# Kernel optimization log

Hardware: AMD Instinct MI355X
Metric: run time of the kernel (lower is better)

Reference implementation:

```python
import jax, jax.numpy as jnp
import numpy as np

D_IN = 2048
D_OUT = 2048
NUM_HEADS = 16
HEAD_DIM = D_OUT // NUM_HEADS
LATENT = 256
B, S = 2, 2048


def setup_inputs() -> dict:
    key = jax.random.key(0)
    ks = jax.random.split(key, 7)
    s = lambda fan_in: 1.0 / np.sqrt(fan_in)
    return {
        "x": jax.random.normal(ks[0], (B, S, D_IN), dtype=jnp.float32),
        "W_query": jax.random.normal(ks[1], (D_IN, D_OUT), dtype=jnp.float32) * s(D_IN),
        "W_DKV": jax.random.normal(ks[2], (D_IN, LATENT), dtype=jnp.float32) * s(D_IN),
        "W_UK": jax.random.normal(ks[3], (LATENT, D_OUT), dtype=jnp.float32) * s(LATENT),
        "W_UV": jax.random.normal(ks[4], (LATENT, D_OUT), dtype=jnp.float32) * s(LATENT),
        "W_out": jax.random.normal(ks[5], (D_OUT, D_OUT), dtype=jnp.float32) * s(D_OUT),
        "b_out": jax.random.normal(ks[6], (D_OUT,), dtype=jnp.float32) * 0.01,
    }


def reference(x, W_query, W_DKV, W_UK, W_UV, W_out, b_out):
    b, n, _ = x.shape
    # projections
    q = x @ W_query                      # [b, n, d_out]
    latent = x @ W_DKV                   # [b, n, latent]
    k = latent @ W_UK                    # [b, n, d_out]
    v = latent @ W_UV                    # [b, n, d_out]
    # split heads -> [b, h, n, hd]
    to_heads = lambda t: t.reshape(b, n, NUM_HEADS, HEAD_DIM).transpose(0, 2, 1, 3)
    q, k, v = to_heads(q), to_heads(k), to_heads(v)
    scores = jnp.einsum("bhqd,bhkd->bhqk", q, k)
    # causal mask: q_pos < k_pos masked to -inf (applied BEFORE scaling, as in source)
    qpos = jnp.arange(n)[:, None]
    kpos = jnp.arange(n)[None, :]
    scores = jnp.where(qpos < kpos, -jnp.inf, scores)
    attn = jax.nn.softmax(scores / np.sqrt(HEAD_DIM), axis=-1)
    ctx = jnp.einsum("bhqk,bhkd->bhqd", attn, v)   # [b, h, n, hd]
    ctx = ctx.transpose(0, 2, 1, 3).reshape(b, n, D_OUT)
    return ctx @ W_out + b_out
```

## Files before the change

### kernel.cpp

```cpp
#include <hip/hip_runtime.h>

#define DIN 2048
#define DOUT 2048
#define NHEADS 16
#define HDIM 128
#define LATENT 256
#define BB 2
#define SS 2048
#define MTOT (BB*SS)

using bf16 = __bf16;
using bf16x8 = __attribute__((ext_vector_type(8))) __bf16;
using f32x4 = __attribute__((ext_vector_type(4))) float;

__device__ __forceinline__ void gload16(const bf16* g, bf16* l) {
    __builtin_amdgcn_global_load_lds(
        (const __attribute__((address_space(1))) void*)g,
        (__attribute__((address_space(3))) void*)l, 16, 0, 0);
}

__global__ void cast_f32_bf16(const float* __restrict__ in, bf16* __restrict__ out, int n) {
    int i = (blockIdx.x * blockDim.x + threadIdx.x) * 8;
    if (i >= n) return;
    float4 a = *(const float4*)(in + i);
    float4 b = *(const float4*)(in + i + 4);
    bf16x8 o;
    o[0] = (bf16)a.x; o[1] = (bf16)a.y; o[2] = (bf16)a.z; o[3] = (bf16)a.w;
    o[4] = (bf16)b.x; o[5] = (bf16)b.y; o[6] = (bf16)b.z; o[7] = (bf16)b.w;
    *(bf16x8*)(out + i) = o;
}

__global__ void transpose_cast(const float* __restrict__ W, bf16* __restrict__ WT, int R, int C) {
    __shared__ float tile[32][33];
    int c0 = blockIdx.x * 32, r0 = blockIdx.y * 32;
    int tx = threadIdx.x & 31, ty = threadIdx.x >> 5;
    #pragma unroll
    for (int i = ty; i < 32; i += 8)
        tile[i][tx] = W[(size_t)(r0 + i) * C + c0 + tx];
    __syncthreads();
    #pragma unroll
    for (int i = ty; i < 32; i += 8)
        WT[(size_t)(c0 + i) * R + r0 + tx] = (bf16)tile[tx][i];
}

__global__ void transpose_v(const bf16* __restrict__ v, bf16* __restrict__ vT) {
    int bh = blockIdx.z;
    int s0 = blockIdx.x * 32, d0 = blockIdx.y * 32;
    __shared__ bf16 t[32][33];
    int tx = threadIdx.x & 31, ty = threadIdx.x >> 5;
    int b = bh >> 4, h = bh & 15;
    #pragma unroll
    for (int i = ty; i < 32; i += 8)
        t[i][tx] = v[(size_t)(b * SS + s0 + i) * DOUT + h * HDIM + d0 + tx];
    __syncthreads();
    #pragma unroll
    for (int i = ty; i < 32; i += 8)
        vT[((size_t)bh * HDIM + d0 + i) * SS + s0 + tx] = t[tx][i];
}

template<bool OUT_F32, bool BIAS>
__global__ __launch_bounds__(256) void gemm_bt(const bf16* __restrict__ A,
        const bf16* __restrict__ BT, void* __restrict__ Cp,
        const float* __restrict__ bias, const int Kdim, const int Ndim) {
    const int n0 = blockIdx.x * 128, m0 = blockIdx.y * 128;
    const int tid = threadIdx.x, wave = tid >> 6, lane = tid & 63;
    const int wm = wave >> 1, wn = wave & 1;
    const int lr = lane & 15, lg = lane >> 4;
    __shared__ __align__(16) bf16 As[128][32];
    __shared__ __align__(16) bf16 Bs[128][32];
    f32x4 acc[4][4];
    #pragma unroll
    for (int i = 0; i < 4; ++i)
        #pragma unroll
        for (int j = 0; j < 4; ++j) acc[i][j] = (f32x4){0.f, 0.f, 0.f, 0.f};

    const int sr = lane >> 2;
    const int sc = (lane & 3) * 8;
    const bf16* ga = A  + (size_t)(m0 + wave * 16 + sr) * Kdim + sc;
    const bf16* gb = BT + (size_t)(n0 + wave * 16 + sr) * Kdim + sc;
    const size_t stride64 = (size_t)64 * Kdim;
    bf16* lAd = &As[wave * 16][0];
    bf16* lBd = &Bs[wave * 16][0];

    for (int k0 = 0; k0 < Kdim; k0 += 32) {
        gload16(ga,            lAd);
        gload16(ga + stride64, lAd + 64 * 32);
        gload16(gb,            lBd);
        gload16(gb + stride64, lBd + 64 * 32);
        ga += 32; gb += 32;
        __syncthreads();
        bf16x8 af[4], bfr[4];
        #pragma unroll
        for (int i = 0; i < 4; ++i)
            af[i] = *(const bf16x8*)&As[wm * 64 + i * 16 + lr][lg * 8];
        #pragma unroll
        for (int j = 0; j < 4; ++j)
            bfr[j] = *(const bf16x8*)&Bs[wn * 64 + j * 16 + lr][lg * 8];
        #pragma unroll
        for (int i = 0; i < 4; ++i)
            #pragma unroll
            for (int j = 0; j < 4; ++j)
                acc[i][j] = __builtin_amdgcn_mfma_f32_16x16x32_bf16(af[i], bfr[j], acc[i][j], 0, 0, 0);
        __syncthreads();
    }
    #pragma unroll
    for (int i = 0; i < 4; ++i)
        #pragma unroll
        for (int j = 0; j < 4; ++j) {
            const int r0 = m0 + wm * 64 + i * 16 + lg * 4;
            const int c = n0 + wn * 64 + j * 16 + lr;
            #pragma unroll
            for (int r2 = 0; r2 < 4; ++r2) {
                float v = acc[i][j][r2];
                if (BIAS) v += bias[c];
                if (OUT_F32) ((float*)Cp)[(size_t)(r0 + r2) * Ndim + c] = v;
                else         ((bf16*)Cp)[(size_t)(r0 + r2) * Ndim + c] = (bf16)v;
            }
        }
}

__global__ __launch_bounds__(256) void attn_kernel(const bf16* __restrict__ q,
        const bf16* __restrict__ k, const bf16* __restrict__ vT, bf16* __restrict__ ctx) {
    const int bh = blockIdx.y, b = bh >> 4, h = bh & 15;
    const int tid = threadIdx.x, wave = tid >> 6, lane = tid & 63;
    const int lr = lane & 15, lg = lane >> 4;
    __shared__ __align__(16) bf16 Ks[64][HDIM + 8];
    __shared__ __align__(16) bf16 Vs[HDIM][64 + 8];
    __shared__ __align__(16) bf16 Ps[64][64 + 8];

    for (int half = 0; half < 2; ++half) {
        const int qt = half ? (31 - (int)blockIdx.x) : (int)blockIdx.x;
        const int q0 = qt * 64;

        bf16x8 qf[4];
        const bf16* qbase = q + ((size_t)(b * SS + q0 + wave * 16 + lr)) * DOUT + h * HDIM;
        #pragma unroll
        for (int d = 0; d < 4; ++d) qf[d] = *(const bf16x8*)(qbase + d * 32 + lg * 8);

        f32x4 o[8];
        #pragma unroll
        for (int i = 0; i < 8; ++i) o[i] = (f32x4){0.f, 0.f, 0.f, 0.f};
        float m_i[4], l_i[4];
        #pragma unroll
        for (int r = 0; r < 4; ++r) { m_i[r] = -__builtin_inff(); l_i[r] = 0.f; }
        const float scale = 0.088388347648318447f;

        const int nkt = qt + 1;
        for (int kt = 0; kt < nkt; ++kt) {
            const int kbase = kt * 64;
            {
                int krow = tid >> 2, kcs = (tid & 3) * 32;
                const bf16* gk = k + ((size_t)(b * SS + kbase + krow)) * DOUT + h * HDIM + kcs;
                #pragma unroll
                for (int u = 0; u < 4; ++u)
                    *(bf16x8*)&Ks[krow][kcs + u * 8] = *(const bf16x8*)(gk + u * 8);
                int vr = tid >> 1, vcs = (tid & 1) * 32;
                const bf16* gv = vT + ((size_t)bh * HDIM + vr) * SS + kbase + vcs;
                #pragma unroll
                for (int u = 0; u < 4; ++u)
                    *(bf16x8*)&Vs[vr][vcs + u * 8] = *(const bf16x8*)(gv + u * 8);
            }
            __syncthreads();

            f32x4 sacc[4];
            #pragma unroll
            for (int nf = 0; nf < 4; ++nf) sacc[nf] = (f32x4){0.f, 0.f, 0.f, 0.f};
            __builtin_amdgcn_s_setprio(1);
            #pragma unroll
            for (int nf = 0; nf < 4; ++nf)
                #pragma unroll
                for (int d = 0; d < 4; ++d) {
                    bf16x8 kf = *(const bf16x8*)&Ks[nf * 16 + lr][d * 32 + lg * 8];
                    sacc[nf] = __builtin_amdgcn_mfma_f32_16x16x32_bf16(qf[d], kf, sacc[nf], 0, 0, 0);
                }
            __builtin_amdgcn_s_setprio(0);

            float sv[4][4];
            const bool maskt = (kbase + 63 > q0);
            #pragma unroll
            for (int nf = 0; nf < 4; ++nf)
                #pragma unroll
                for (int r = 0; r < 4; ++r) {
                    float s = sacc[nf][r] * scale;
                    if (maskt) {
                        int qr = q0 + wave * 16 + lg * 4 + r;
                        int kc = kbase + nf * 16 + lr;
                        if (qr < kc) s = -__builtin_inff();
                    }
                    sv[nf][r] = s;
                }
            float corr[4];
            #pragma unroll
            for (int r = 0; r < 4; ++r) {
                float v = fmaxf(fmaxf(sv[0][r], sv[1][r]), fmaxf(sv[2][r], sv[3][r]));
                #pragma unroll
                for (int off = 1; off < 16; off <<= 1) v = fmaxf(v, __shfl_xor(v, off));
                float mnew = fmaxf(m_i[r], v);
                corr[r] = __expf(m_i[r] - mnew);
                m_i[r] = mnew;
            }
            float rsum[4] = {0.f, 0.f, 0.f, 0.f};
            #pragma unroll
            for (int nf = 0; nf < 4; ++nf)
                #pragma unroll
                for (int r = 0; r < 4; ++r) {
                    float p = __expf(sv[nf][r] - m_i[r]);
                    rsum[r] += p;
                    Ps[wave * 16 + lg * 4 + r][nf * 16 + lr] = (bf16)p;
                }
            #pragma unroll
            for (int r = 0; r < 4; ++r) {
                float v = rsum[r];
                #pragma unroll
                for (int off = 1; off < 16; off <<= 1) v += __shfl_xor(v, off);
                l_i[r] = l_i[r] * corr[r] + v;
            }
            #pragma unroll
            for (int df = 0; df < 8; ++df)
                #pragma unroll
                for (int r = 0; r < 4; ++r) o[df][r] *= corr[r];

            __builtin_amdgcn_s_setprio(1);
            #pragma unroll
            for (int ks = 0; ks < 2; ++ks) {
                bf16x8 pf = *(const bf16x8*)&Ps[wave * 16 + lr][ks * 32 + lg * 8];
                #pragma unroll
                for (int df = 0; df < 8; ++df) {
                    bf16x8 vf = *(const bf16x8*)&Vs[df * 16 + lr][ks * 32 + lg * 8];
                    o[df] = __builtin_amdgcn_mfma_f32_16x16x32_bf16(pf, vf, o[df], 0, 0, 0);
                }
            }
            __builtin_amdgcn_s_setprio(0);
            __syncthreads();
        }

        #pragma unroll
        for (int df = 0; df < 8; ++df)
            #pragma unroll
            for (int r = 0; r < 4; ++r) {
                int rrow = q0 + wave * 16 + lg * 4 + r;
                int col = h * HDIM + df * 16 + lr;
                ctx[(size_t)(b * SS + rrow) * DOUT + col] = (bf16)(o[df][r] / l_i[r]);
            }
    }
}

extern "C" void kernel_launch(void* const* d_in, const int* in_sizes, int n_in,
                              void* d_out, int out_size, void* d_ws, size_t ws_size,
                              hipStream_t stream) {
    const float* x    = (const float*)d_in[0];
    const float* Wq   = (const float*)d_in[1];
    const float* Wdkv = (const float*)d_in[2];
    const float* Wuk  = (const float*)d_in[3];
    const float* Wuv  = (const float*)d_in[4];
    const float* Wout = (const float*)d_in[5];
    const float* bout = (const float*)d_in[6];

    char* ws = (char*)d_ws;
    size_t off = 0;
    auto alloc = [&](size_t bytes) { char* p = ws + off; off = (off + bytes + 255) & ~255ULL; return p; };
    bf16* xb    = (bf16*)alloc((size_t)MTOT * DIN * 2);
    bf16* WqT   = (bf16*)alloc((size_t)DOUT * DIN * 2);
    bf16* WdkvT = (bf16*)alloc((size_t)LATENT * DIN * 2);
    bf16* WukT  = (bf16*)alloc((size_t)DOUT * LATENT * 2);
    bf16* WuvT  = (bf16*)alloc((size_t)DOUT * LATENT * 2);
    bf16* WoutT = (bf16*)alloc((size_t)DOUT * DOUT * 2);
    bf16* qb    = (bf16*)alloc((size_t)MTOT * DOUT * 2);
    bf16* lat   = (bf16*)alloc((size_t)MTOT * LATENT * 2);
    bf16* kb    = (bf16*)alloc((size_t)MTOT * DOUT * 2);
    bf16* vb    = (bf16*)alloc((size_t)MTOT * DOUT * 2);
    bf16* vT    = (bf16*)alloc((size_t)BB * NHEADS * HDIM * SS * 2);
    bf16* ctx   = (bf16*)alloc((size_t)MTOT * DOUT * 2);

    cast_f32_bf16<<<(MTOT * DIN) / 8 / 256, 256, 0, stream>>>(x, xb, MTOT * DIN);
    transpose_cast<<<dim3(DOUT / 32, DIN / 32), 256, 0, stream>>>(Wq, WqT, DIN, DOUT);
    transpose_cast<<<dim3(LATENT / 32, DIN / 32), 256, 0, stream>>>(Wdkv, WdkvT, DIN, LATENT);
    transpose_cast<<<dim3(DOUT / 32, LATENT / 32), 256, 0, stream>>>(Wuk, WukT, LATENT, DOUT);
    transpose_cast<<<dim3(DOUT / 32, LATENT / 32), 256, 0, stream>>>(Wuv, WuvT, LATENT, DOUT);
    transpose_cast<<<dim3(DOUT / 32, DOUT / 32), 256, 0, stream>>>(Wout, WoutT, DOUT, DOUT);

    gemm_bt<false, false><<<dim3(DOUT / 128, MTOT / 128), 256, 0, stream>>>(xb, WqT, qb, nullptr, DIN, DOUT);
    gemm_bt<false, false><<<dim3(LATENT / 128, MTOT / 128), 256, 0, stream>>>(xb, WdkvT, lat, nullptr, DIN, LATENT);
    gemm_bt<false, false><<<dim3(DOUT / 128, MTOT / 128), 256, 0, stream>>>(lat, WukT, kb, nullptr, LATENT, DOUT);
    gemm_bt<false, false><<<dim3(DOUT / 128, MTOT / 128), 256, 0, stream>>>(lat, WuvT, vb, nullptr, LATENT, DOUT);

    transpose_v<<<dim3(SS / 32, HDIM / 32, BB * NHEADS), 256, 0, stream>>>(vb, vT);

    attn_kernel<<<dim3(16, BB * NHEADS), 256, 0, stream>>>(qb, kb, vT, ctx);

    gemm_bt<true, true><<<dim3(DOUT / 128, MTOT / 128), 256, 0, stream>>>(ctx, WoutT, d_out, bout, DOUT, DOUT);
}
```

Measured before the change: 428.5 us.

## Fuse projection GEMMs, prefetch K/V in attention, swizzle LDS and block order

Merges the Q and latent projections into one GEMM, and the K and V up-projections into another, by relying on the transposed weights sitting contiguously in the workspace. The GEMM now takes separate leading dimensions so it can read and write the strided fused buffers. The attention kernel gains register prefetch of the next K/V tile, XOR-swizzled LDS layouts to avoid bank conflicts, and exp2 with the softmax scale folded in. Both kernels also remap block order with an XCD-style swizzle. The intent is fewer launches, better L2 locality and less LDS and latency stall, at the cost of relying on the workspace layout and on a finite -3e38 mask value.

```diff
diff --git a/kernel.cpp b/kernel.cpp
--- a/kernel.cpp
+++ b/kernel.cpp
@@ -8,6 +8,8 @@
 #define BB 2
 #define SS 2048
 #define MTOT (BB*SS)
+#define QLD (DOUT + LATENT)
+#define KLD (2*DOUT)
 
 using bf16 = __bf16;
 using bf16x8 = __attribute__((ext_vector_type(8))) __bf16;
@@ -51,7 +53,7 @@
     int b = bh >> 4, h = bh & 15;
     #pragma unroll
     for (int i = ty; i < 32; i += 8)
-        t[i][tx] = v[(size_t)(b * SS + s0 + i) * DOUT + h * HDIM + d0 + tx];
+        t[i][tx] = v[(size_t)(b * SS + s0 + i) * KLD + h * HDIM + d0 + tx];
     __syncthreads();
     #pragma unroll
     for (int i = ty; i < 32; i += 8)
@@ -61,8 +63,13 @@
 template<bool OUT_F32, bool BIAS>
 __global__ __launch_bounds__(256) void gemm_bt(const bf16* __restrict__ A,
         const bf16* __restrict__ BT, void* __restrict__ Cp,
-        const float* __restrict__ bias, const int Kdim, const int Ndim) {
-    const int n0 = blockIdx.x * 128, m0 = blockIdx.y * 128;
+        const float* __restrict__ bias, const int Kdim, const int Ald,
+        const int Ndim, const int Cld) {
+    const int nwg = gridDim.x * gridDim.y;
+    int orig = blockIdx.y * gridDim.x + blockIdx.x;
+    int swz = (orig & 7) * (nwg >> 3) + (orig >> 3);
+    const int n0 = (swz % gridDim.x) * 128, m0 = (swz / gridDim.x) * 128;
+
     const int tid = threadIdx.x, wave = tid >> 6, lane = tid & 63;
     const int wm = wave >> 1, wn = wave & 1;
     const int lr = lane & 15, lg = lane >> 4;
@@ -76,17 +83,18 @@
 
     const int sr = lane >> 2;
     const int sc = (lane & 3) * 8;
-    const bf16* ga = A  + (size_t)(m0 + wave * 16 + sr) * Kdim + sc;
+    const bf16* ga = A  + (size_t)(m0 + wave * 16 + sr) * Ald + sc;
     const bf16* gb = BT + (size_t)(n0 + wave * 16 + sr) * Kdim + sc;
-    const size_t stride64 = (size_t)64 * Kdim;
+    const size_t strideA64 = (size_t)64 * Ald;
+    const size_t strideB64 = (size_t)64 * Kdim;
     bf16* lAd = &As[wave * 16][0];
     bf16* lBd = &Bs[wave * 16][0];
 
     for (int k0 = 0; k0 < Kdim; k0 += 32) {
-        gload16(ga,            lAd);
-        gload16(ga + stride64, lAd + 64 * 32);
-        gload16(gb,            lBd);
-        gload16(gb + stride64, lBd + 64 * 32);
+        gload16(ga,             lAd);
+        gload16(ga + strideA64, lAd + 64 * 32);
+        gload16(gb,             lBd);
+        gload16(gb + strideB64, lBd + 64 * 32);
         ga += 32; gb += 32;
         __syncthreads();
         bf16x8 af[4], bfr[4];
@@ -113,27 +121,46 @@
             for (int r2 = 0; r2 < 4; ++r2) {
                 float v = acc[i][j][r2];
                 if (BIAS) v += bias[c];
-                if (OUT_F32) ((float*)Cp)[(size_t)(r0 + r2) * Ndim + c] = v;
-                else         ((bf16*)Cp)[(size_t)(r0 + r2) * Ndim + c] = (bf16)v;
+                if (OUT_F32) ((float*)Cp)[(size_t)(r0 + r2) * Cld + c] = v;
+                else         ((bf16*)Cp)[(size_t)(r0 + r2) * Cld + c] = (bf16)v;
             }
         }
 }
 
 __global__ __launch_bounds__(256) void attn_kernel(const bf16* __restrict__ q,
         const bf16* __restrict__ k, const bf16* __restrict__ vT, bf16* __restrict__ ctx) {
-    const int bh = blockIdx.y, b = bh >> 4, h = bh & 15;
+    int orig = blockIdx.y * 16 + blockIdx.x;
+    int swz = (orig & 7) * 64 + (orig >> 3);
+    const int bx = swz & 15, bh = swz >> 4;
+    const int b = bh >> 4, h = bh & 15;
     const int tid = threadIdx.x, wave = tid >> 6, lane = tid & 63;
     const int lr = lane & 15, lg = lane >> 4;
-    __shared__ __align__(16) bf16 Ks[64][HDIM + 8];
-    __shared__ __align__(16) bf16 Vs[HDIM][64 + 8];
-    __shared__ __align__(16) bf16 Ps[64][64 + 8];
+
+    __shared__ __align__(16) bf16 KsL[64 * 128];
+    __shared__ __align__(16) bf16 VsL[128 * 64];
+    __shared__ __align__(16) bf16 PsL[64 * 64];
+
+    char* KsB = (char*)KsL; char* VsB = (char*)VsL; char* PsB = (char*)PsL;
+
+    const int krow = tid >> 2, kc0b = (tid & 3) * 64;
+    const int vrow = tid >> 1, vc0b = (tid & 1) * 64;
+    int kOff[4], vOff[4];
+    #pragma unroll
+    for (int u = 0; u < 4; ++u) {
+        kOff[u] = (krow * 256 + kc0b + u * 16) ^ ((krow & 7) << 4);
+        vOff[u] = (vrow * 128 + vc0b + u * 16) ^ ((vrow & 7) << 4);
+    }
+    const bf16* gkb = k  + ((size_t)b * SS + krow) * KLD + h * HDIM + (tid & 3) * 32;
+    const bf16* gvb = vT + ((size_t)bh * HDIM + vrow) * SS + (tid & 1) * 32;
+
+    const float C = 0.12751744f;
 
     for (int half = 0; half < 2; ++half) {
-        const int qt = half ? (31 - (int)blockIdx.x) : (int)blockIdx.x;
+        const int qt = half ? (31 - bx) : bx;
         const int q0 = qt * 64;
 
         bf16x8 qf[4];
-        const bf16* qbase = q + ((size_t)(b * SS + q0 + wave * 16 + lr)) * DOUT + h * HDIM;
+        const bf16* qbase = q + ((size_t)(b * SS + q0 + wave * 16 + lr)) * QLD + h * HDIM;
         #pragma unroll
         for (int d = 0; d < 4; ++d) qf[d] = *(const bf16x8*)(qbase + d * 32 + lg * 8);
 
@@ -142,25 +169,34 @@
         for (int i = 0; i < 8; ++i) o[i] = (f32x4){0.f, 0.f, 0.f, 0.f};
         float m_i[4], l_i[4];
         #pragma unroll
-        for (int r = 0; r < 4; ++r) { m_i[r] = -__builtin_inff(); l_i[r] = 0.f; }
-        const float scale = 0.088388347648318447f;
+        for (int r = 0; r < 4; ++r) { m_i[r] = -3.0e38f; l_i[r] = 0.f; }
 
         const int nkt = qt + 1;
+        bf16x8 kreg[4], vreg[4];
+        #pragma unroll
+        for (int u = 0; u < 4; ++u) {
+            kreg[u] = *(const bf16x8*)(gkb + (size_t)0 * 64 * KLD + u * 8);
+            vreg[u] = *(const bf16x8*)(gvb + 0 * 64 + u * 8);
+        }
+        #pragma unroll
+        for (int u = 0; u < 4; ++u) {
+            *(bf16x8*)(KsB + kOff[u]) = kreg[u];
+            *(bf16x8*)(VsB + vOff[u]) = vreg[u];
+        }
+        __syncthreads();
+
         for (int kt = 0; kt < nkt; ++kt) {
             const int kbase = kt * 64;
-            {
-                int krow = tid >> 2, kcs = (tid & 3) * 32;
-                const bf16* gk = k + ((size_t)(b * SS + kbase + krow)) * DOUT + h * HDIM + kcs;
-                #pragma unroll
-                for (int u = 0; u < 4; ++u)
-                    *(bf16x8*)&Ks[krow][kcs + u * 8] = *(const bf16x8*)(gk + u * 8);
-                int vr = tid >> 1, vcs = (tid & 1) * 32;
-                const bf16* gv = vT + ((size_t)bh * HDIM + vr) * SS + kbase + vcs;
-                #pragma unroll
-                for (int u = 0; u < 4; ++u)
-                    *(bf16x8*)&Vs[vr][vcs + u * 8] = *(const bf16x8*)(gv + u * 8);
-            }
-            __syncthreads();
+            const bool have_next = (kt + 1 < nkt);
+            if (have_next) {
+                const bf16* gk = gkb + (size_t)(kt + 1) * 64 * KLD;
+                const bf16* gv = gvb + (kt + 1) * 64;
+                #pragma unroll
+                for (int u = 0; u < 4; ++u) {
+                    kreg[u] = *(const bf16x8*)(gk + u * 8);
+                    vreg[u] = *(const bf16x8*)(gv + u * 8);
+                }
+            }
 
             f32x4 sacc[4];
             #pragma unroll
@@ -170,7 +206,8 @@
             for (int nf = 0; nf < 4; ++nf)
                 #pragma unroll
                 for (int d = 0; d < 4; ++d) {
-                    bf16x8 kf = *(const bf16x8*)&Ks[nf * 16 + lr][d * 32 + lg * 8];
+                    int row = nf * 16 + lr;
+                    bf16x8 kf = *(const bf16x8*)(KsB + ((row * 256 + d * 64 + lg * 16) ^ ((row & 7) << 4)));
                     sacc[nf] = __builtin_amdgcn_mfma_f32_16x16x32_bf16(qf[d], kf, sacc[nf], 0, 0, 0);
                 }
             __builtin_amdgcn_s_setprio(0);
@@ -181,11 +218,11 @@
             for (int nf = 0; nf < 4; ++nf)
                 #pragma unroll
                 for (int r = 0; r < 4; ++r) {
-                    float s = sacc[nf][r] * scale;
+                    float s = sacc[nf][r];
                     if (maskt) {
                         int qr = q0 + wave * 16 + lg * 4 + r;
                         int kc = kbase + nf * 16 + lr;
-                        if (qr < kc) s = -__builtin_inff();
+                        if (qr < kc) s = -3.0e38f;
                     }
                     sv[nf][r] = s;
                 }
@@ -196,7 +233,7 @@
                 #pragma unroll
                 for (int off = 1; off < 16; off <<= 1) v = fmaxf(v, __shfl_xor(v, off));
                 float mnew = fmaxf(m_i[r], v);
-                corr[r] = __expf(m_i[r] - mnew);
+                corr[r] = __builtin_amdgcn_exp2f((m_i[r] - mnew) * C);
                 m_i[r] = mnew;
             }
             float rsum[4] = {0.f, 0.f, 0.f, 0.f};
@@ -204,9 +241,10 @@
             for (int nf = 0; nf < 4; ++nf)
                 #pragma unroll
                 for (int r = 0; r < 4; ++r) {
-                    float p = __expf(sv[nf][r] - m_i[r]);
+                    float p = __builtin_amdgcn_exp2f((sv[nf][r] - m_i[r]) * C);
                     rsum[r] += p;
-                    Ps[wave * 16 + lg * 4 + r][nf * 16 + lr] = (bf16)p;
+                    int prow = wave * 16 + lg * 4 + r;
+                    *(bf16*)(PsB + ((prow * 128 + (nf * 16 + lr) * 2) ^ ((prow & 7) << 4))) = (bf16)p;
                 }
             #pragma unroll
             for (int r = 0; r < 4; ++r) {
@@ -223,25 +261,37 @@
             __builtin_amdgcn_s_setprio(1);
             #pragma unroll
             for (int ks = 0; ks < 2; ++ks) {
-                bf16x8 pf = *(const bf16x8*)&Ps[wave * 16 + lr][ks * 32 + lg * 8];
+                int prow = wave * 16 + lr;
+                bf16x8 pf = *(const bf16x8*)(PsB + ((prow * 128 + ks * 64 + lg * 16) ^ ((prow & 7) << 4)));
                 #pragma unroll
                 for (int df = 0; df < 8; ++df) {
-                    bf16x8 vf = *(const bf16x8*)&Vs[df * 16 + lr][ks * 32 + lg * 8];
+                    int vr2 = df * 16 + lr;
+                    bf16x8 vf = *(const bf16x8*)(VsB + ((vr2 * 128 + ks * 64 + lg * 16) ^ ((vr2 & 7) << 4)));
                     o[df] = __builtin_amdgcn_mfma_f32_16x16x32_bf16(pf, vf, o[df], 0, 0, 0);
                 }
             }
             __builtin_amdgcn_s_setprio(0);
             __syncthreads();
-        }
-
-        #pragma unroll
-        for (int df = 0; df < 8; ++df)
-            #pragma unroll
-            for (int r = 0; r < 4; ++r) {
+            if (have_next) {
+                #pragma unroll
+                for (int u = 0; u < 4; ++u) {
+                    *(bf16x8*)(KsB + kOff[u]) = kreg[u];
+                    *(bf16x8*)(VsB + vOff[u]) = vreg[u];
+                }
+            }
+            __syncthreads();
+        }
+
+        #pragma unroll
+        for (int r = 0; r < 4; ++r) {
+            float inv = 1.0f / l_i[r];
+            #pragma unroll
+            for (int df = 0; df < 8; ++df) {
                 int rrow = q0 + wave * 16 + lg * 4 + r;
                 int col = h * HDIM + df * 16 + lr;
-                ctx[(size_t)(b * SS + rrow) * DOUT + col] = (bf16)(o[df][r] / l_i[r]);
-            }
+                ctx[(size_t)(b * SS + rrow) * DOUT + col] = (bf16)(o[df][r] * inv);
+            }
+        }
     }
 }
 
@@ -265,10 +315,8 @@
     bf16* WukT  = (bf16*)alloc((size_t)DOUT * LATENT * 2);
     bf16* WuvT  = (bf16*)alloc((size_t)DOUT * LATENT * 2);
     bf16* WoutT = (bf16*)alloc((size_t)DOUT * DOUT * 2);
-    bf16* qb    = (bf16*)alloc((size_t)MTOT * DOUT * 2);
-    bf16* lat   = (bf16*)alloc((size_t)MTOT * LATENT * 2);
-    bf16* kb    = (bf16*)alloc((size_t)MTOT * DOUT * 2);
-    bf16* vb    = (bf16*)alloc((size_t)MTOT * DOUT * 2);
+    bf16* qlat  = (bf16*)alloc((size_t)MTOT * QLD * 2);
+    bf16* kvb   = (bf16*)alloc((size_t)MTOT * KLD * 2);
     bf16* vT    = (bf16*)alloc((size_t)BB * NHEADS * HDIM * SS * 2);
     bf16* ctx   = (bf16*)alloc((size_t)MTOT * DOUT * 2);
 
@@ -279,14 +327,15 @@
     transpose_cast<<<dim3(DOUT / 32, LATENT / 32), 256, 0, stream>>>(Wuv, WuvT, LATENT, DOUT);
     transpose_cast<<<dim3(DOUT / 32, DOUT / 32), 256, 0, stream>>>(Wout, WoutT, DOUT, DOUT);
 
-    gemm_bt<false, false><<<dim3(DOUT / 128, MTOT / 128), 256, 0, stream>>>(xb, WqT, qb, nullptr, DIN, DOUT);
-    gemm_bt<false, false><<<dim3(LATENT / 128, MTOT / 128), 256, 0, stream>>>(xb, WdkvT, lat, nullptr, DIN, LATENT);
-    gemm_bt<false, false><<<dim3(DOUT / 128, MTOT / 128), 256, 0, stream>>>(lat, WukT, kb, nullptr, LATENT, DOUT);
-    gemm_bt<false, false><<<dim3(DOUT / 128, MTOT / 128), 256, 0, stream>>>(lat, WuvT, vb, nullptr, LATENT, DOUT);
-
-    transpose_v<<<dim3(SS / 32, HDIM / 32, BB * NHEADS), 256, 0, stream>>>(vb, vT);
-
-    attn_kernel<<<dim3(16, BB * NHEADS), 256, 0, stream>>>(qb, kb, vT, ctx);
-
-    gemm_bt<true, true><<<dim3(DOUT / 128, MTOT / 128), 256, 0, stream>>>(ctx, WoutT, d_out, bout, DOUT, DOUT);
-}
+    gemm_bt<false, false><<<dim3(QLD / 128, MTOT / 128), 256, 0, stream>>>(
+        xb, WqT, qlat, nullptr, DIN, DIN, QLD, QLD);
+    gemm_bt<false, false><<<dim3(KLD / 128, MTOT / 128), 256, 0, stream>>>(
+        qlat + DOUT, WukT, kvb, nullptr, LATENT, QLD, KLD, KLD);
+
+    transpose_v<<<dim3(SS / 32, HDIM / 32, BB * NHEADS), 256, 0, stream>>>(kvb + DOUT, vT);
+
+    attn_kernel<<<dim3(16, BB * NHEADS), 256, 0, stream>>>(qlat, kvb, vT, ctx);
+
+    gemm_bt<true, true><<<dim3(DOUT / 128, MTOT / 128), 256, 0, stream>>>(
+        ctx, WoutT, d_out, bout, DOUT, DOUT, DOUT, DOUT);
+}
```

New measurement: 444.7 us. 3.8% more time.
